# Kernel tuning notes

Hardware: AMD Instinct MI355X
Metric: run time of the kernel (lower is better)

Reference implementation:

```python
import jax, jax.numpy as jnp
import numpy as np


def _unfold(x, k):
    # x: [B, C, H, W] -> [B, C, S, L] with S=k*k (row-major patch order), L=H*W
    B, C, H, W = x.shape
    pad = k // 2
    xp = jnp.pad(x, ((0, 0), (0, 0), (pad, pad), (pad, pad)))
    patches = jnp.stack(
        [xp[:, :, r:r + H, c:c + W] for r in range(k) for c in range(k)], axis=2
    )  # [B, C, S, H, W]
    return patches.reshape(B, C, k * k, H * W)


def setup_inputs() -> dict:
    key = jax.random.key(0)
    ks = jax.random.split(key, 8)
    B, C, H, W = 8, 64, 128, 128
    R, Cout = 4, 128
    x = jax.random.normal(ks[0], (B, C, H, W), dtype=jnp.float32)
    gate_w = jax.random.normal(ks[1], (R, C), dtype=jnp.float32) * 0.05   # 1x1 gate conv weight
    gate_b = jax.random.normal(ks[2], (R,), dtype=jnp.float32) * 0.01
    theta = jax.random.normal(ks[3], (R,), dtype=jnp.float32) * 0.5       # learned directions
    raw_sigma_u = jax.random.normal(ks[4], (R,), dtype=jnp.float32) * 0.1
    raw_sigma_s = jax.random.normal(ks[5], (R,), dtype=jnp.float32) * 0.1
    pw_w = jax.random.normal(ks[6], (Cout, R * C), dtype=jnp.float32) * (1.0 / np.sqrt(R * C).astype(np.float32))
    pw_b = jax.random.normal(ks[7], (Cout,), dtype=jnp.float32) * 0.01
    return {"x": x, "gate_w": gate_w, "gate_b": gate_b, "theta": theta,
            "raw_sigma_u": raw_sigma_u, "raw_sigma_s": raw_sigma_s,
            "pw_w": pw_w, "pw_b": pw_b}


def reference(x, gate_w, gate_b, theta, raw_sigma_u, raw_sigma_s, pw_w, pw_b):
    k = 3
    B, C, H, W = x.shape
    R = theta.shape[0]
    S, L = k * k, H * W

    x_un = _unfold(x, k)                                         # [B, C, S, L]

    # 1x1 gate conv + fuzzy softmax over rules
    logits = jnp.einsum('bchw,rc->brhw', x, gate_w) + gate_b[None, :, None, None]
    mu = jax.nn.softmax(logits, axis=1)                          # [B, R, H, W]
    mu_un = _unfold(mu, k)                                       # [B, R, S, L]
    s_center = (k // 2) * k + (k // 2)
    mu_center = mu_un[:, :, s_center:s_center + 1, :]            # [B, R, 1, L]

    # anisotropic Gaussian kernel per rule over integer offsets (row-major)
    grid = np.arange(k, dtype=np.float32) - k // 2
    dy = jnp.asarray(np.repeat(grid, k))                         # [S]
    dx = jnp.asarray(np.tile(grid, k))                           # [S]
    cos_t, sin_t = jnp.cos(theta)[:, None], jnp.sin(theta)[:, None]
    proj_u = cos_t * dx[None, :] + sin_t * dy[None, :]           # [R, S]
    proj_s = -sin_t * dx[None, :] + cos_t * dy[None, :]
    su = (jax.nn.softplus(raw_sigma_u) + 1e-4)[:, None]
    ss = (jax.nn.softplus(raw_sigma_s) + 1e-4)[:, None]
    kern = jnp.exp(-proj_u ** 2 / su ** 2 - proj_s ** 2 / ss ** 2)  # [R, S]

    alpha = mu_center * mu_un * kern[None, :, :, None]           # [B, R, S, L]
    alpha_sum = jnp.maximum(alpha.sum(axis=(1, 2), keepdims=True), 1e-8)
    alpha = alpha / alpha_sum

    agg = jnp.einsum('brsl,bcsl->brcl', alpha, x_un)             # [B, R, C, L]
    agg_flat = agg.reshape(B, R * C, L)
    out = jnp.einsum('bnl,on->bol', agg_flat, pw_w) + pw_b[None, :, None]
    return out.reshape(B, -1, H, W)
```

## Files before the change

### kernel.cpp

```cpp
#include <hip/hip_runtime.h>
#include <math.h>

#define CC 64
#define RR 4
#define HH 128
#define WW 128
#define BB 8
#define COUT 128
#define XST 68
#define ALS 44
#define AGS 268

typedef __attribute__((ext_vector_type(8))) short short8;
typedef __attribute__((ext_vector_type(4))) short short4v;
typedef __attribute__((ext_vector_type(4))) float f32x4;
typedef __attribute__((ext_vector_type(2))) float f32x2;

__device__ __forceinline__ unsigned short f2bf(float f) {
  unsigned u = __float_as_uint(f);
  u += 0x7fffu + ((u >> 16) & 1u);
  return (unsigned short)(u >> 16);
}
__device__ __forceinline__ float bf2f(unsigned short h) {
  return __uint_as_float(((unsigned)h) << 16);
}
__device__ __forceinline__ float blo(unsigned u) { return __uint_as_float(u << 16); }
__device__ __forceinline__ float bhi(unsigned u) { return __uint_as_float(u & 0xffff0000u); }

__global__ __launch_bounds__(256) void k_pre(const float* __restrict__ theta,
                                             const float* __restrict__ rsu,
                                             const float* __restrict__ rss,
                                             const float* __restrict__ pw,
                                             const float* __restrict__ gw,
                                             float* __restrict__ wkern,
                                             unsigned short* __restrict__ pwb,
                                             unsigned short* __restrict__ gwb) {
  int i = blockIdx.x * 256 + threadIdx.x;
  if (i < COUT * RR * CC) pwb[i] = f2bf(pw[i]);
  if (blockIdx.x == 0 && threadIdx.x < RR * 9) {
    int t = threadIdx.x;
    int r = t / 9, s = t % 9;
    float dy = (float)(s / 3 - 1), dx = (float)(s % 3 - 1);
    float ct = cosf(theta[r]), st = sinf(theta[r]);
    float su = log1pf(expf(rsu[r])) + 1e-4f;
    float sv = log1pf(expf(rss[r])) + 1e-4f;
    float pu = ct * dx + st * dy;
    float ps = -st * dx + ct * dy;
    wkern[t] = expf(-(pu * pu) / (su * su) - (ps * ps) / (sv * sv));
  }
  if (blockIdx.x == 1) {
    #pragma unroll
    for (int k = 0; k < 4; ++k) {
      int j = k * 256 + threadIdx.x;
      gwb[j] = (j < RR * CC) ? f2bf(gw[j]) : (unsigned short)0;
    }
  }
}

__global__ __launch_bounds__(512, 4) void k_fused(const float* __restrict__ x,
                                                  const float* __restrict__ gb,
                                                  const float* __restrict__ wkern,
                                                  const unsigned short* __restrict__ pwb,
                                                  const unsigned short* __restrict__ gwb,
                                                  const float* __restrict__ pb,
                                                  float* __restrict__ out) {
  __shared__ unsigned short xsT[240][XST];
  __shared__ unsigned short mus[RR][6][40];
  __shared__ unsigned short alp[128][ALS];
  __shared__ float rsum[RR][128];
  __shared__ __align__(16) unsigned short aggs[32][AGS];

  int tid = threadIdx.x;
  int raw = blockIdx.x;
  int bid = (raw & 7) * 128 + (raw >> 3);
  int b = bid >> 7;
  int rem = bid & 127;
  int h0 = (rem >> 2) << 2;
  int w0 = (rem & 3) << 5;

  int lane = tid & 63;
  int wv = tid >> 6;
  int lr = lane & 15, lq = lane >> 4;
  int o0 = wv << 4;

  short8 a0r[8];
  {
    const unsigned short* pA = pwb + ((o0 + lr) << 8) + (lq << 3);
    #pragma unroll
    for (int ks = 0; ks < 8; ++ks) a0r[ks] = *(const short8*)(pA + (ks << 5));
  }
  short8 am0 = *(const short8*)(gwb + (lr << 6) + (lq << 3));
  short8 am1 = *(const short8*)(gwb + (lr << 6) + 32 + (lq << 3));
  float4 pbv = *(const float4*)&pb[o0 + (lq << 2)];
  float gb0 = gb[0], gb1 = gb[1], gb2 = gb[2], gb3 = gb[3];

  #pragma unroll
  for (int k = 0; k < 2; ++k) {
    int item = k * 512 + tid;
    if (item < 960) {
      int c4 = item % 10;
      int rest = item / 10;
      int cquad = rest / 6;
      int row = rest - cquad * 6;
      int c = cquad << 2;
      int gcol = w0 - 4 + (c4 << 2);
      int grow = h0 - 1 + row;
      float4 v0 = make_float4(0.f,0.f,0.f,0.f), v1 = v0, v2 = v0, v3 = v0;
      if ((unsigned)gcol < WW && (unsigned)grow < HH) {
        const float* xp = x + (((size_t)b * CC + c) << 14) + (grow << 7) + gcol;
        v0 = *(const float4*)xp;
        v1 = *(const float4*)(xp + (1 << 14));
        v2 = *(const float4*)(xp + (2 << 14));
        v3 = *(const float4*)(xp + (3 << 14));
      }
      int spb = row * 40 + (c4 << 2);
      float4 vv[4] = {v0, v1, v2, v3};
      #pragma unroll
      for (int j = 0; j < 4; ++j) {
        int sp = spb + j;
        float f0 = (&vv[0].x)[j], f1 = (&vv[1].x)[j], f2v = (&vv[2].x)[j], f3 = (&vv[3].x)[j];
        ushort4 uv;
        uv.x = f2bf(f0); uv.y = f2bf(f1); uv.z = f2bf(f2v); uv.w = f2bf(f3);
        *(ushort4*)&xsT[sp][c] = uv;
      }
    }
  }
  __syncthreads();

  for (int j = wv; j < 13; j += 8) {
    int p = (j << 4) + lr;
    int pcl = p > 203 ? 203 : p;
    unsigned y = (unsigned)pcl / 34u;
    int cxo = pcl - (int)(y * 34u);
    int pos = (int)y * 40 + 3 + cxo;
    short4v b0l = *(const short4v*)&xsT[pos][lq << 3];
    short4v b0h = *(const short4v*)&xsT[pos][(lq << 3) + 4];
    short4v b1l = *(const short4v*)&xsT[pos][32 + (lq << 3)];
    short4v b1h = *(const short4v*)&xsT[pos][32 + (lq << 3) + 4];
    short8 b0 = __builtin_shufflevector(b0l, b0h, 0,1,2,3,4,5,6,7);
    short8 b1 = __builtin_shufflevector(b1l, b1h, 0,1,2,3,4,5,6,7);
    f32x4 mac = (f32x4){0.f, 0.f, 0.f, 0.f};
    mac = __builtin_amdgcn_mfma_f32_16x16x32_bf16(am0, b0, mac, 0, 0, 0);
    mac = __builtin_amdgcn_mfma_f32_16x16x32_bf16(am1, b1, mac, 0, 0, 0);
    if (lq == 0 && p < 204) {
      int grow = h0 - 1 + (int)y, gcol = w0 - 1 + cxo;
      float lg0 = mac[0] + gb0, lg1 = mac[1] + gb1;
      float lg2 = mac[2] + gb2, lg3 = mac[3] + gb3;
      float m = fmaxf(fmaxf(lg0, lg1), fmaxf(lg2, lg3));
      float e0 = expf(lg0 - m), e1 = expf(lg1 - m);
      float e2 = expf(lg2 - m), e3 = expf(lg3 - m);
      float inv = 1.0f / (e0 + e1 + e2 + e3);
      if (!((unsigned)grow < HH && (unsigned)gcol < WW)) inv = 0.0f;
      mus[0][y][3 + cxo] = f2bf(e0 * inv);
      mus[1][y][3 + cxo] = f2bf(e1 * inv);
      mus[2][y][3 + cxo] = f2bf(e2 * inv);
      mus[3][y][3 + cxo] = f2bf(e3 * inv);
    }
  }
  __syncthreads();

  {
    int t = tid & 127, r = tid >> 7;
    int prow = t >> 5, pcol = t & 31;
    float mc = bf2f(mus[r][prow + 1][pcol + 4]);
    float sum = 0.f;
    #pragma unroll
    for (int s = 0; s < 9; ++s) {
      float av = mc * bf2f(mus[r][prow + s / 3][pcol + 3 + s % 3]) * wkern[r * 9 + s];
      alp[t][(s << 2) + r] = f2bf(av);
      sum += av;
    }
    rsum[r][t] = sum;
  }
  __syncthreads();

  for (int rd = 0; rd < 4; ++rd) {
    {
      int t = tid & 31, cg = tid >> 5;
      int px = (rd << 5) + t;
      float inv = 1.0f / fmaxf(rsum[0][px] + rsum[1][px] + rsum[2][px] + rsum[3][px], 1e-8f);

      uint2 ad[9];
      #pragma unroll
      for (int s = 0; s < 9; ++s) ad[s] = *(const uint2*)(&alp[px][s << 2]);

      f32x2 cacc[4][2];
      #pragma unroll
      for (int r = 0; r < 4; ++r) {
        cacc[r][0] = (f32x2){0.f, 0.f};
        cacc[r][1] = (f32x2){0.f, 0.f};
      }

      int c0 = cg << 2;
      #pragma unroll
      for (int s = 0; s < 9; ++s) {
        int sp = (rd + s / 3) * 40 + t + 3 + s % 3;
        uint2 ux = *(const uint2*)&xsT[sp][c0];
        f32x2 xv0 = {blo(ux.x), bhi(ux.x)};
        f32x2 xv1 = {blo(ux.y), bhi(ux.y)};
        unsigned adx = ad[s].x, ady = ad[s].y;
        float af0 = blo(adx), af1 = bhi(adx), af2 = blo(ady), af3 = bhi(ady);
        f32x2 A0 = {af0, af0}, A1 = {af1, af1}, A2 = {af2, af2}, A3 = {af3, af3};
        cacc[0][0] += A0 * xv0; cacc[0][1] += A0 * xv1;
        cacc[1][0] += A1 * xv0; cacc[1][1] += A1 * xv1;
        cacc[2][0] += A2 * xv0; cacc[2][1] += A2 * xv1;
        cacc[3][0] += A3 * xv0; cacc[3][1] += A3 * xv1;
      }
      #pragma unroll
      for (int r = 0; r < 4; ++r) {
        ushort4 wvv;
        wvv.x = f2bf(cacc[r][0][0] * inv); wvv.y = f2bf(cacc[r][0][1] * inv);
        wvv.z = f2bf(cacc[r][1][0] * inv); wvv.w = f2bf(cacc[r][1][1] * inv);
        *(ushort4*)&aggs[t][(r << 6) + c0] = wvv;
      }
    }
    __syncthreads();

    {
      f32x4 dacc0 = (f32x4){0.f, 0.f, 0.f, 0.f};
      f32x4 dacc1 = (f32x4){0.f, 0.f, 0.f, 0.f};
      #pragma unroll
      for (int ks = 0; ks < 8; ++ks) {
        int off = (ks << 5) + (lq << 3);
        short4v l0 = *(const short4v*)&aggs[lr][off];
        short4v h0 = *(const short4v*)&aggs[lr][off + 4];
        short4v l1 = *(const short4v*)&aggs[16 + lr][off];
        short4v h1 = *(const short4v*)&aggs[16 + lr][off + 4];
        short8 b0 = __builtin_shufflevector(l0, h0, 0,1,2,3,4,5,6,7);
        short8 b1 = __builtin_shufflevector(l1, h1, 0,1,2,3,4,5,6,7);
        dacc0 = __builtin_amdgcn_mfma_f32_16x16x32_bf16(a0r[ks], b0, dacc0, 0, 0, 0);
        dacc1 = __builtin_amdgcn_mfma_f32_16x16x32_bf16(a0r[ks], b1, dacc1, 0, 0, 0);
      }
      int orow = h0 + rd;
      #pragma unroll
      for (int q = 0; q < 4; ++q) {
        int o = o0 + (lq << 2) + q;
        size_t base = (((size_t)b * COUT + o) << 14) + (orow << 7) + w0;
        out[base + lr]      = dacc0[q] + pbv[q];
        out[base + 16 + lr] = dacc1[q] + pbv[q];
      }
    }
    if (rd < 3) __syncthreads();
  }
}

extern "C" void kernel_launch(void* const* d_in, const int* in_sizes, int n_in,
                              void* d_out, int out_size, void* d_ws, size_t ws_size,
                              hipStream_t stream) {
  const float* x     = (const float*)d_in[0];
  const float* gw    = (const float*)d_in[1];
  const float* gb    = (const float*)d_in[2];
  const float* theta = (const float*)d_in[3];
  const float* rsu   = (const float*)d_in[4];
  const float* rss   = (const float*)d_in[5];
  const float* pw    = (const float*)d_in[6];
  const float* pb    = (const float*)d_in[7];
  float* outp = (float*)d_out;

  float* wkern = (float*)d_ws;
  unsigned short* pwb = (unsigned short*)(wkern + 64);
  unsigned short* gwb = pwb + COUT * RR * CC;

  k_pre<<<128, 256, 0, stream>>>(theta, rsu, rss, pw, gw, wkern, pwb, gwb);
  k_fused<<<BB * (HH / 4) * (WW / 32), 512, 0, stream>>>(x, gb, wkern, pwb, gwb, pb, outp);
}
```

Baseline: 49.13 us.

## Double-buffer aggregation tile to overlap aggregation with MFMA projection

Splits the aggregation stage into 16-pixel chunks written to a double-buffered shared tile, so the next chunk's aggregation is computed before the MFMA projection of the current chunk. This removes one barrier per stage pair and lets the VALU aggregation interleave with the matrix work. Each thread now handles 2 channels instead of 4, and launch bounds drop from 4 to 2 blocks per CU, which frees registers but may lower occupancy. The loop is also fully unrolled over 8 half-rows, which increases code size.

```diff
diff --git a/kernel.cpp b/kernel.cpp
--- a/kernel.cpp
+++ b/kernel.cpp
@@ -57,7 +57,7 @@
   }
 }
 
-__global__ __launch_bounds__(512, 4) void k_fused(const float* __restrict__ x,
+__global__ __launch_bounds__(512, 2) void k_fused(const float* __restrict__ x,
                                                   const float* __restrict__ gb,
                                                   const float* __restrict__ wkern,
                                                   const unsigned short* __restrict__ pwb,
@@ -68,7 +68,7 @@
   __shared__ unsigned short mus[RR][6][40];
   __shared__ unsigned short alp[128][ALS];
   __shared__ float rsum[RR][128];
-  __shared__ __align__(16) unsigned short aggs[32][AGS];
+  __shared__ __align__(16) unsigned short aggs[2][16][AGS];
 
   int tid = threadIdx.x;
   int raw = blockIdx.x;
@@ -174,73 +174,70 @@
   }
   __syncthreads();
 
-  for (int rd = 0; rd < 4; ++rd) {
-    {
-      int t = tid & 31, cg = tid >> 5;
-      int px = (rd << 5) + t;
-      float inv = 1.0f / fmaxf(rsum[0][px] + rsum[1][px] + rsum[2][px] + rsum[3][px], 1e-8f);
-
-      uint2 ad[9];
-      #pragma unroll
-      for (int s = 0; s < 9; ++s) ad[s] = *(const uint2*)(&alp[px][s << 2]);
-
-      f32x2 cacc[4][2];
-      #pragma unroll
-      for (int r = 0; r < 4; ++r) {
-        cacc[r][0] = (f32x2){0.f, 0.f};
-        cacc[r][1] = (f32x2){0.f, 0.f};
-      }
-
-      int c0 = cg << 2;
-      #pragma unroll
-      for (int s = 0; s < 9; ++s) {
-        int sp = (rd + s / 3) * 40 + t + 3 + s % 3;
-        uint2 ux = *(const uint2*)&xsT[sp][c0];
-        f32x2 xv0 = {blo(ux.x), bhi(ux.x)};
-        f32x2 xv1 = {blo(ux.y), bhi(ux.y)};
-        unsigned adx = ad[s].x, ady = ad[s].y;
-        float af0 = blo(adx), af1 = bhi(adx), af2 = blo(ady), af3 = bhi(ady);
-        f32x2 A0 = {af0, af0}, A1 = {af1, af1}, A2 = {af2, af2}, A3 = {af3, af3};
-        cacc[0][0] += A0 * xv0; cacc[0][1] += A0 * xv1;
-        cacc[1][0] += A1 * xv0; cacc[1][1] += A1 * xv1;
-        cacc[2][0] += A2 * xv0; cacc[2][1] += A2 * xv1;
-        cacc[3][0] += A3 * xv0; cacc[3][1] += A3 * xv1;
-      }
-      #pragma unroll
-      for (int r = 0; r < 4; ++r) {
-        ushort4 wvv;
-        wvv.x = f2bf(cacc[r][0][0] * inv); wvv.y = f2bf(cacc[r][0][1] * inv);
-        wvv.z = f2bf(cacc[r][1][0] * inv); wvv.w = f2bf(cacc[r][1][1] * inv);
-        *(ushort4*)&aggs[t][(r << 6) + c0] = wvv;
-      }
-    }
-    __syncthreads();
-
-    {
-      f32x4 dacc0 = (f32x4){0.f, 0.f, 0.f, 0.f};
-      f32x4 dacc1 = (f32x4){0.f, 0.f, 0.f, 0.f};
-      #pragma unroll
-      for (int ks = 0; ks < 8; ++ks) {
-        int off = (ks << 5) + (lq << 3);
-        short4v l0 = *(const short4v*)&aggs[lr][off];
-        short4v h0 = *(const short4v*)&aggs[lr][off + 4];
-        short4v l1 = *(const short4v*)&aggs[16 + lr][off];
-        short4v h1 = *(const short4v*)&aggs[16 + lr][off + 4];
-        short8 b0 = __builtin_shufflevector(l0, h0, 0,1,2,3,4,5,6,7);
-        short8 b1 = __builtin_shufflevector(l1, h1, 0,1,2,3,4,5,6,7);
-        dacc0 = __builtin_amdgcn_mfma_f32_16x16x32_bf16(a0r[ks], b0, dacc0, 0, 0, 0);
-        dacc1 = __builtin_amdgcn_mfma_f32_16x16x32_bf16(a0r[ks], b1, dacc1, 0, 0, 0);
-      }
-      int orow = h0 + rd;
+  int t16 = tid & 15;
+  int cg = tid >> 4;
+  int c0 = cg << 1;
+
+  auto phaseC = [&](int rd2) {
+    unsigned short (*ab)[AGS] = aggs[rd2 & 1];
+    int px = (rd2 << 4) + t16;
+    int prow2 = px >> 5, pc = px & 31;
+    float inv = 1.0f / fmaxf(rsum[0][px] + rsum[1][px] + rsum[2][px] + rsum[3][px], 1e-8f);
+    f32x2 cacc0 = (f32x2){0.f, 0.f}, cacc1 = cacc0, cacc2 = cacc0, cacc3 = cacc0;
+    #pragma unroll
+    for (int s = 0; s < 9; ++s) {
+      int sp = (prow2 + s / 3) * 40 + pc + 3 + s % 3;
+      unsigned ux = *(const unsigned*)&xsT[sp][c0];
+      f32x2 xv = {blo(ux), bhi(ux)};
+      uint2 adv = *(const uint2*)&alp[px][s << 2];
+      float af0 = blo(adv.x), af1 = bhi(adv.x), af2 = blo(adv.y), af3 = bhi(adv.y);
+      cacc0 += (f32x2){af0, af0} * xv;
+      cacc1 += (f32x2){af1, af1} * xv;
+      cacc2 += (f32x2){af2, af2} * xv;
+      cacc3 += (f32x2){af3, af3} * xv;
+    }
+    ushort2 w0v, w1v, w2v, w3v;
+    w0v.x = f2bf(cacc0[0] * inv); w0v.y = f2bf(cacc0[1] * inv);
+    w1v.x = f2bf(cacc1[0] * inv); w1v.y = f2bf(cacc1[1] * inv);
+    w2v.x = f2bf(cacc2[0] * inv); w2v.y = f2bf(cacc2[1] * inv);
+    w3v.x = f2bf(cacc3[0] * inv); w3v.y = f2bf(cacc3[1] * inv);
+    *(ushort2*)&ab[t16][c0]       = w0v;
+    *(ushort2*)&ab[t16][64 + c0]  = w1v;
+    *(ushort2*)&ab[t16][128 + c0] = w2v;
+    *(ushort2*)&ab[t16][192 + c0] = w3v;
+  };
+
+  phaseC(0);
+  __syncthreads();
+
+  f32x4 dprev = (f32x4){0.f, 0.f, 0.f, 0.f};
+  #pragma unroll
+  for (int rd = 0; rd < 8; ++rd) {
+    if (rd < 7) phaseC(rd + 1);
+
+    const unsigned short (*ab)[AGS] = aggs[rd & 1];
+    f32x4 dacc = (f32x4){0.f, 0.f, 0.f, 0.f};
+    #pragma unroll
+    for (int ks = 0; ks < 8; ++ks) {
+      int off = (ks << 5) + (lq << 3);
+      short4v l0 = *(const short4v*)&ab[lr][off];
+      short4v h0 = *(const short4v*)&ab[lr][off + 4];
+      short8 b0 = __builtin_shufflevector(l0, h0, 0,1,2,3,4,5,6,7);
+      dacc = __builtin_amdgcn_mfma_f32_16x16x32_bf16(a0r[ks], b0, dacc, 0, 0, 0);
+    }
+    if ((rd & 1) == 0) {
+      dprev = dacc;
+    } else {
+      int orow = h0 + (rd >> 1);
       #pragma unroll
       for (int q = 0; q < 4; ++q) {
         int o = o0 + (lq << 2) + q;
         size_t base = (((size_t)b * COUT + o) << 14) + (orow << 7) + w0;
-        out[base + lr]      = dacc0[q] + pbv[q];
-        out[base + 16 + lr] = dacc1[q] + pbv[q];
+        out[base + lr]      = dprev[q] + pbv[q];
+        out[base + 16 + lr] = dacc[q] + pbv[q];
       }
     }
-    if (rd < 3) __syncthreads();
+    if (rd < 7) __syncthreads();
   }
 }
 
```

Result: slower. 50.29 us (+2.4%).
